# Optimization experiments

Hardware: AMD Instinct MI355X
Metric: run time of the kernel (lower is better)

Reference implementation:

```python
import jax, jax.numpy as jnp
from jax import lax
import numpy as np

D_MODEL = 1024
EXP = 2
D_INNER = EXP * D_MODEL
D_STATE = 16
D_CONV = 4
DT_RANK = 64  # ceil(d_model/16), mamba default
NUM_GROUPS = 4
BSZ, SEQ = 2, 2048
EPS = 1e-5


def setup_inputs() -> dict:
    key = jax.random.key(0)
    ks = jax.random.split(key, 10)
    def n(k, shape, s=0.02):
        return jax.random.normal(k, shape, jnp.float32) * s
    return dict(
        x=jax.random.normal(ks[0], (BSZ, SEQ, D_MODEL), jnp.float32),
        ln1_g=jnp.ones((D_MODEL,), jnp.float32), ln1_b=jnp.zeros((D_MODEL,), jnp.float32),
        ln2_g=jnp.ones((D_MODEL,), jnp.float32), ln2_b=jnp.zeros((D_MODEL,), jnp.float32),
        W1=n(ks[1], (EXP * D_MODEL, D_MODEL)), b1=jnp.zeros((EXP * D_MODEL,), jnp.float32),
        W2=n(ks[2], (D_MODEL, EXP * D_MODEL)), b2=jnp.zeros((D_MODEL,), jnp.float32),
        in_proj_w=n(ks[3], (2 * D_INNER, D_MODEL)),
        conv_w=n(ks[4], (D_INNER, 1, D_CONV), 0.2), conv_b=jnp.zeros((D_INNER,), jnp.float32),
        x_proj_w=n(ks[5], (DT_RANK + 2 * D_STATE, D_INNER)),
        dt_proj_w=n(ks[6], (D_INNER, DT_RANK), 0.1), dt_proj_b=n(ks[7], (D_INNER,), 0.5),
        A_log=jnp.tile(jnp.log(jnp.arange(1, D_STATE + 1, dtype=jnp.float32)), (D_INNER, 1)),
        D_param=jnp.ones((D_INNER,), jnp.float32),
        out_proj_w=n(ks[8], (D_MODEL, D_INNER)),
    )


def _layernorm(x, g, b):
    m = jnp.mean(x, -1, keepdims=True)
    v = jnp.var(x, -1, keepdims=True)
    return (x - m) * lax.rsqrt(v + EPS) * g + b


def _ste_sign(w):
    # sign quantization with straight-through estimator (groupwise split is a no-op for sign)
    return w + lax.stop_gradient(jnp.sign(w) - w)


def _quant_act_groupwise(x, b=8):
    # groups along seq dim (x.shape[1]); gamma is the abs-max over the whole group slab
    Qb = float(2 ** (b - 1))
    B_, L, D = x.shape
    g = x.reshape(B_, NUM_GROUPS, L // NUM_GROUPS, D)
    gamma = jnp.max(jnp.abs(g), axis=(0, 2, 3), keepdims=True)
    q = jnp.clip(g * Qb / (gamma + EPS), -Qb + EPS, Qb - EPS)
    return q.reshape(B_, L, D)


def _mamba(u, in_proj_w, conv_w, conv_b, x_proj_w, dt_proj_w, dt_proj_b, A_log, D_param, out_proj_w):
    B_, L, _ = u.shape
    xz = u @ in_proj_w.T                         # [B, L, 2*d_inner]
    xs, z = jnp.split(xz, 2, axis=-1)
    # depthwise causal conv1d
    xt = jnp.transpose(xs, (0, 2, 1))            # [B, d_inner, L]
    xt = lax.conv_general_dilated(xt, conv_w, (1,), [(D_CONV - 1, 0)],
                                  feature_group_count=D_INNER,
                                  dimension_numbers=('NCH', 'OIH', 'NCH'))
    xt = xt + conv_b[None, :, None]
    xs = jax.nn.silu(jnp.transpose(xt, (0, 2, 1)))  # [B, L, d_inner]
    x_dbl = xs @ x_proj_w.T                      # [B, L, dt_rank + 2*d_state]
    dt, Bm, Cm = jnp.split(x_dbl, [DT_RANK, DT_RANK + D_STATE], axis=-1)
    dt = jax.nn.softplus(dt @ dt_proj_w.T + dt_proj_b)   # [B, L, d_inner]
    A = -jnp.exp(A_log)                          # [d_inner, d_state]

    def step(h, inp):
        dt_s, B_s, C_s, x_s = inp                # [B,di], [B,ds], [B,ds], [B,di]
        dA = jnp.exp(dt_s[..., None] * A)        # [B, di, ds]
        h = h * dA + (dt_s * x_s)[..., None] * B_s[:, None, :]
        y = jnp.einsum('bds,bs->bd', h, C_s)
        return h, y

    tm = lambda a: jnp.transpose(a, (1, 0, 2))   # time-major
    h0 = jnp.zeros((B_, D_INNER, D_STATE), u.dtype)
    _, ys = lax.scan(step, h0, (tm(dt), tm(Bm), tm(Cm), tm(xs)))
    y = jnp.transpose(ys, (1, 0, 2)) + D_param * xs
    y = y * jax.nn.silu(z)
    return y @ out_proj_w.T


def reference(x, ln1_g, ln1_b, ln2_g, ln2_b, W1, b1, W2, b2,
              in_proj_w, conv_w, conv_b, x_proj_w, dt_proj_w, dt_proj_b,
              A_log, D_param, out_proj_w):
    qW1 = _ste_sign(W1)
    qW2 = _ste_sign(W2)
    gated = jnp.clip(_layernorm(x, ln1_g, ln1_b) @ qW1.T + b1, -1.0, 1.0)  # Hardtanh
    x = x + gated @ qW2.T + b2
    qx = _quant_act_groupwise(x)
    out = qx + _mamba(_layernorm(qx, ln2_g, ln2_b), in_proj_w, conv_w, conv_b,
                      x_proj_w, dt_proj_w, dt_proj_b, A_log, D_param, out_proj_w)
    return out
```

## Files before the change

kernel.cpp:

```cpp
#include <hip/hip_runtime.h>
#include <math.h>

#define D_MODEL 1024
#define D_INNER 2048
#define D_STATE 16
#define DT_RANK 64
#define BSZ 2
#define SEQ 2048
#define NTOK (BSZ*SEQ)
#define NCH  (BSZ*D_INNER)
#define NCHUNK 64
#define CLEN 32
#define EPS 1e-5f

typedef __attribute__((ext_vector_type(8))) short short8v;
typedef __attribute__((ext_vector_type(4))) float f32x4;

__device__ __forceinline__ float sgnf(float w) {
    return (w > 0.f) ? 1.f : ((w < 0.f) ? -1.f : 0.f);
}
__device__ __forceinline__ unsigned short f2bf(float f) {
    unsigned int x = __float_as_uint(f);
    x += 0x7fffu + ((x >> 16) & 1u);
    return (unsigned short)(x >> 16);
}
__device__ __forceinline__ float bf2f(unsigned short u) {
    return __uint_as_float(((unsigned int)u) << 16);
}
__device__ __forceinline__ void stage16(const unsigned short* g, unsigned short* l) {
    __builtin_amdgcn_global_load_lds(
        (const __attribute__((address_space(1))) unsigned int*)g,
        (__attribute__((address_space(3))) unsigned int*)l, 16, 0, 0);
}

#define F4_C1   524288
#define F4_C2   1048576
#define F4_C3   2097152
#define F4_C4   2146304
#define F4_C5   2179072
#define F4_C6   2703360
__global__ __launch_bounds__(256) void f2bf_all_kernel(
    const float* __restrict__ W1, const float* __restrict__ W2,
    const float* __restrict__ inpj, const float* __restrict__ xpj,
    const float* __restrict__ dtpj, const float* __restrict__ outpj,
    unsigned short* __restrict__ o_w1, unsigned short* __restrict__ o_w2,
    unsigned short* __restrict__ o_in, unsigned short* __restrict__ o_xp,
    unsigned short* __restrict__ o_dt, unsigned short* __restrict__ o_out,
    unsigned int* __restrict__ gma)
{
    int i = blockIdx.x * 256 + threadIdx.x;
    if (blockIdx.x == 0 && threadIdx.x < 4) gma[threadIdx.x] = 0u;
    if (i >= F4_C6) return;
    const float* src; unsigned short* dst; int off; bool sign = false;
    if (i < F4_C1)      { src = W1;   dst = o_w1;  off = i;          sign = true; }
    else if (i < F4_C2) { src = W2;   dst = o_w2;  off = i - F4_C1;  sign = true; }
    else if (i < F4_C3) { src = inpj; dst = o_in;  off = i - F4_C2; }
    else if (i < F4_C4) { src = xpj;  dst = o_xp;  off = i - F4_C3; }
    else if (i < F4_C5) { src = dtpj; dst = o_dt;  off = i - F4_C4; }
    else                { src = outpj;dst = o_out; off = i - F4_C5; }
    float4 v = reinterpret_cast<const float4*>(src)[off];
    if (sign) { v.x = sgnf(v.x); v.y = sgnf(v.y); v.z = sgnf(v.z); v.w = sgnf(v.w); }
    ushort4 o;
    o.x = f2bf(v.x); o.y = f2bf(v.y); o.z = f2bf(v.z); o.w = f2bf(v.w);
    reinterpret_cast<ushort4*>(dst)[off] = o;
}

__global__ __launch_bounds__(256) void ln_hilo_kernel(const float* __restrict__ x,
                                                      const float* __restrict__ g,
                                                      const float* __restrict__ b,
                                                      unsigned short* __restrict__ hi,
                                                      unsigned short* __restrict__ lo) {
    int row = blockIdx.x, tid = threadIdx.x;
    float4 v = reinterpret_cast<const float4*>(x + (size_t)row * D_MODEL)[tid];
    float s = v.x + v.y + v.z + v.w;
    float q = v.x*v.x + v.y*v.y + v.z*v.z + v.w*v.w;
    #pragma unroll
    for (int off = 32; off > 0; off >>= 1) { s += __shfl_down(s, off); q += __shfl_down(q, off); }
    __shared__ float rs[4], rq[4], smean, srstd;
    if ((tid & 63) == 0) { rs[tid >> 6] = s; rq[tid >> 6] = q; }
    __syncthreads();
    if (tid == 0) {
        float ts = rs[0]+rs[1]+rs[2]+rs[3], tq = rq[0]+rq[1]+rq[2]+rq[3];
        float mean = ts * (1.0f / D_MODEL);
        smean = mean;
        srstd = rsqrtf(tq * (1.0f / D_MODEL) - mean*mean + EPS);
    }
    __syncthreads();
    float mean = smean, rstd = srstd;
    float4 gg = reinterpret_cast<const float4*>(g)[tid];
    float4 bb = reinterpret_cast<const float4*>(b)[tid];
    float o[4];
    o[0] = (v.x-mean)*rstd*gg.x + bb.x; o[1] = (v.y-mean)*rstd*gg.y + bb.y;
    o[2] = (v.z-mean)*rstd*gg.z + bb.z; o[3] = (v.w-mean)*rstd*gg.w + bb.w;
    ushort4 h4, l4;
    h4.x = f2bf(o[0]); l4.x = f2bf(o[0] - bf2f(h4.x));
    h4.y = f2bf(o[1]); l4.y = f2bf(o[1] - bf2f(h4.y));
    h4.z = f2bf(o[2]); l4.z = f2bf(o[2] - bf2f(h4.z));
    h4.w = f2bf(o[3]); l4.w = f2bf(o[3] - bf2f(h4.w));
    reinterpret_cast<ushort4*>(hi + (size_t)row * D_MODEL)[tid] = h4;
    reinterpret_cast<ushort4*>(lo + (size_t)row * D_MODEL)[tid] = l4;
}

template<int EP, bool DUALA, int BN, bool KSPLIT>
__global__ __launch_bounds__(256) void mfma_gemm(
    const unsigned short* __restrict__ A, const unsigned short* __restrict__ A2,
    const unsigned short* __restrict__ B, float* __restrict__ C,
    unsigned short* __restrict__ Cb,
    int M, int N, int K, int sA, int sC,
    const float* __restrict__ bias, const float* __restrict__ addx, int sAdd,
    unsigned int* __restrict__ gma, int ksl)
{
    constexpr int NF = BN / 32;
    __shared__ __align__(16) unsigned short As[128*32];
    __shared__ __align__(16) unsigned short As2[DUALA ? 128*32 : 8];
    __shared__ __align__(16) unsigned short Bs[BN*32];
    __shared__ float redmax[4];
    const int tid = threadIdx.x;
    const int lane = tid & 63;
    const int w = tid >> 6;
    const int wm = w >> 1, wn = w & 1;

    int bx = blockIdx.x, by = blockIdx.y;
    if (!KSPLIT) {
        const int gx = gridDim.x;
        const int nwg = gx * gridDim.y;
        int lin = by * gx + bx;
        int nl = (lin & 7) * (nwg >> 3) + (lin >> 3);
        bx = nl % gx; by = nl / gx;
    }
    const int row0 = by * 128, col0 = bx * BN;
    const int srow = lane >> 2;
    const int scol = (lane & 3) * 8;

    int k_begin = 0, k_end = K;
    if (KSPLIT) {
        int z = blockIdx.z;
        k_begin = z * ksl; k_end = k_begin + ksl;
        C += (size_t)z * M * sC;
    }

    f32x4 acc[4][NF];
    #pragma unroll
    for (int m = 0; m < 4; ++m)
        #pragma unroll
        for (int n = 0; n < NF; ++n)
            acc[m][n] = (f32x4){0.f, 0.f, 0.f, 0.f};

    for (int k0 = k_begin; k0 < k_end; k0 += 32) {
        #pragma unroll
        for (int i = 0; i < 2; ++i) {
            const int rbase = w * 32 + i * 16;
            stage16(A + (size_t)(row0 + rbase + srow) * sA + k0 + scol, &As[rbase * 32]);
            if (DUALA)
                stage16(A2 + (size_t)(row0 + rbase + srow) * sA + k0 + scol, &As2[rbase * 32]);
        }
        #pragma unroll
        for (int i = 0; i < BN/64; ++i) {
            const int rbase = (BN == 128) ? (w * 32 + i * 16) : (w * 16);
            if (col0 + rbase < N)
                stage16(B + (size_t)(col0 + rbase + srow) * K + k0 + scol, &Bs[rbase * 32]);
        }
        __syncthreads();

        short8v af[4], bfr[NF], af2[4];
        const int fr = lane & 15, kg = (lane >> 4) * 8;
        #pragma unroll
        for (int m = 0; m < 4; ++m)
            af[m] = *reinterpret_cast<const short8v*>(&As[(wm*64 + m*16 + fr) * 32 + kg]);
        if (DUALA) {
            #pragma unroll
            for (int m = 0; m < 4; ++m)
                af2[m] = *reinterpret_cast<const short8v*>(&As2[(wm*64 + m*16 + fr) * 32 + kg]);
        }
        #pragma unroll
        for (int n = 0; n < NF; ++n)
            bfr[n] = *reinterpret_cast<const short8v*>(&Bs[(wn*(BN/2) + n*16 + fr) * 32 + kg]);

        #pragma unroll
        for (int m = 0; m < 4; ++m)
            #pragma unroll
            for (int n = 0; n < NF; ++n) {
                acc[m][n] = __builtin_amdgcn_mfma_f32_16x16x32_bf16(af[m], bfr[n], acc[m][n], 0, 0, 0);
                if (DUALA)
                    acc[m][n] = __builtin_amdgcn_mfma_f32_16x16x32_bf16(af2[m], bfr[n], acc[m][n], 0, 0, 0);
            }
        __syncthreads();
    }

    const int fc = lane & 15, r4 = (lane >> 4) * 4;
    float lmax = 0.0f;
    #pragma unroll
    for (int m = 0; m < 4; ++m) {
        const int grb = row0 + wm*64 + m*16 + r4;
        #pragma unroll
        for (int n = 0; n < NF; ++n) {
            const int gc = col0 + wn*(BN/2) + n*16 + fc;
            if (gc >= N) continue;
            #pragma unroll
            for (int j = 0; j < 4; ++j) {
                const int r = grb + j;
                float v = acc[m][n][j];
                if (EP == 0) {
                    C[(size_t)r*sC + gc] = v;
                } else if (EP == 1) {
                    v += bias[gc];
                    v = fminf(1.0f, fmaxf(-1.0f, v));
                    Cb[(size_t)r*sC + gc] = f2bf(v);
                } else if (EP == 3) {
                    float t = v + bias[gc];
                    t = fmaxf(t, 0.0f) + log1pf(__expf(-fabsf(t)));
                    Cb[(size_t)r*sC + gc] = f2bf(t);
                } else if (EP == 4) {
                    C[(size_t)r*sC + gc] = v + addx[(size_t)r*sAdd + gc];
                } else if (EP == 6) {
                    Cb[(size_t)r*sC + gc] = f2bf(v);
                } else {
                    v += bias[gc] + addx[(size_t)r*sAdd + gc];
                    C[(size_t)r*sC + gc] = v;
                    lmax = fmaxf(lmax, fabsf(v));
                }
            }
        }
    }
    if (EP == 7) {
        #pragma unroll
        for (int off = 32; off > 0; off >>= 1) lmax = fmaxf(lmax, __shfl_down(lmax, off));
        if (lane == 0) redmax[w] = lmax;
        __syncthreads();
        if (tid == 0) {
            float t = fmaxf(fmaxf(redmax[0], redmax[1]), fmaxf(redmax[2], redmax[3]));
            int g = (row0 & (SEQ - 1)) >> 9;
            atomicMax(gma + g, __float_as_uint(t));
        }
    }
}

__global__ __launch_bounds__(256) void xproj_combine_kernel(
    const float* __restrict__ part,
    float* __restrict__ xdbl,
    unsigned short* __restrict__ xdt)
{
    int i = blockIdx.x * 256 + threadIdx.x;
    if (i >= NTOK * 24) return;
    const size_t stride = (size_t)NTOK * 96 / 4;
    float4 v0 = reinterpret_cast<const float4*>(part)[i];
    float4 v1 = reinterpret_cast<const float4*>(part)[i + stride];
    float4 v2 = reinterpret_cast<const float4*>(part)[i + 2*stride];
    float4 v3 = reinterpret_cast<const float4*>(part)[i + 3*stride];
    float4 o;
    o.x = (v0.x + v1.x) + (v2.x + v3.x);
    o.y = (v0.y + v1.y) + (v2.y + v3.y);
    o.z = (v0.z + v1.z) + (v2.z + v3.z);
    o.w = (v0.w + v1.w) + (v2.w + v3.w);
    reinterpret_cast<float4*>(xdbl)[i] = o;
    int row = i / 24, c4 = i % 24;
    if (c4 < 16) {
        ushort4 u;
        u.x = f2bf(o.x); u.y = f2bf(o.y); u.z = f2bf(o.z); u.w = f2bf(o.w);
        reinterpret_cast<ushort4*>(xdt + (size_t)row * 64)[c4] = u;
    }
}

__global__ __launch_bounds__(256) void quant_ln_kernel(
    const float* __restrict__ x2, const unsigned int* __restrict__ gamma_bits,
    const float* __restrict__ g, const float* __restrict__ b,
    float* __restrict__ qx, unsigned short* __restrict__ u)
{
    int row = blockIdx.x, tid = threadIdx.x;
    int grp = (row & (SEQ - 1)) >> 9;
    float gamma = __uint_as_float(gamma_bits[grp]);
    float scale = 128.0f / (gamma + EPS);
    const float lo = -128.0f + EPS, hi = 128.0f - EPS;
    float4 v = reinterpret_cast<const float4*>(x2 + (size_t)row * D_MODEL)[tid];
    float4 qv;
    qv.x = fminf(hi, fmaxf(lo, v.x * scale));
    qv.y = fminf(hi, fmaxf(lo, v.y * scale));
    qv.z = fminf(hi, fmaxf(lo, v.z * scale));
    qv.w = fminf(hi, fmaxf(lo, v.w * scale));
    reinterpret_cast<float4*>(qx + (size_t)row * D_MODEL)[tid] = qv;
    float s = qv.x + qv.y + qv.z + qv.w;
    float q = qv.x*qv.x + qv.y*qv.y + qv.z*qv.z + qv.w*qv.w;
    #pragma unroll
    for (int off = 32; off > 0; off >>= 1) { s += __shfl_down(s, off); q += __shfl_down(q, off); }
    __shared__ float rs[4], rq[4], smean, srstd;
    if ((tid & 63) == 0) { rs[tid >> 6] = s; rq[tid >> 6] = q; }
    __syncthreads();
    if (tid == 0) {
        float ts = rs[0]+rs[1]+rs[2]+rs[3], tq = rq[0]+rq[1]+rq[2]+rq[3];
        float mean = ts * (1.0f / D_MODEL);
        smean = mean;
        srstd = rsqrtf(tq * (1.0f / D_MODEL) - mean*mean + EPS);
    }
    __syncthreads();
    float mean = smean, rstd = srstd;
    float4 gg = reinterpret_cast<const float4*>(g)[tid];
    float4 bb = reinterpret_cast<const float4*>(b)[tid];
    ushort4 o;
    o.x = f2bf((qv.x-mean)*rstd*gg.x + bb.x);
    o.y = f2bf((qv.y-mean)*rstd*gg.y + bb.y);
    o.z = f2bf((qv.z-mean)*rstd*gg.z + bb.z);
    o.w = f2bf((qv.w-mean)*rstd*gg.w + bb.w);
    reinterpret_cast<ushort4*>(u + (size_t)row * D_MODEL)[tid] = o;
}

__global__ __launch_bounds__(256) void conv_silu_kernel(const unsigned short* __restrict__ xz,
                                                        const float* __restrict__ conv_w,
                                                        const float* __restrict__ conv_b,
                                                        unsigned short* __restrict__ xcb) {
    int c = blockIdx.x * 256 + threadIdx.x;
    int m = blockIdx.y;
    int b = m >> 11, l = m & (SEQ - 1);
    float4 w4 = reinterpret_cast<const float4*>(conv_w)[c];
    float wv[4] = {w4.x, w4.y, w4.z, w4.w};
    float s = conv_b[c];
    const unsigned short* base = xz + ((size_t)b * SEQ) * 4096 + c;
    #pragma unroll
    for (int k = 0; k < 4; ++k) {
        int ll = l - 3 + k;
        if (ll >= 0) s += bf2f(base[(size_t)ll * 4096]) * wv[k];
    }
    float sig = 1.0f / (1.0f + __expf(-s));
    xcb[(size_t)m * D_INNER + c] = f2bf(s * sig);
}

__device__ __forceinline__ void make_dA(float dA[D_STATE], float dtv,
                                        const float* a, bool pw) {
    if (pw) {
        dA[0] = __expf(dtv * a[0]);
        #pragma unroll
        for (int s = 1; s < D_STATE; ++s) dA[s] = dA[s>>1] * dA[(s-1)>>1];
    } else {
        #pragma unroll
        for (int s = 0; s < D_STATE; ++s) dA[s] = __expf(dtv * a[s]);
    }
}

__global__ __launch_bounds__(256) void scan_partial_kernel(
    const unsigned short* __restrict__ dt, const unsigned short* __restrict__ xcb,
    const float* __restrict__ xdbl, const float* __restrict__ A_log,
    float* __restrict__ Lbuf, float* __restrict__ Sbuf)
{
    int gtid = blockIdx.x * 256 + threadIdx.x;
    int ch = gtid & (NCH - 1);
    int c  = gtid >> 12;
    int b = ch >> 11, d = ch & (D_INNER - 1);
    float a[D_STATE], h[D_STATE];
    bool pw = true;
    #pragma unroll
    for (int s = 0; s < D_STATE; ++s) {
        a[s] = -__expf(A_log[(size_t)d * D_STATE + s]);
        h[s] = 0.0f;
    }
    #pragma unroll
    for (int s = 1; s < D_STATE; ++s)
        pw = pw && (fabsf(a[s] - a[0]*(float)(s+1)) <= 1e-3f * fabsf(a[s]));

    size_t m0 = (size_t)b * SEQ + (size_t)c * CLEN;
    float Ssum = 0.0f;

    float dt_n = bf2f(dt[m0 * D_INNER + d]);
    float x_n  = bf2f(xcb[m0 * D_INNER + d]);
    float4 B_n[4];
    {
        const float* xd = xdbl + m0 * 96;
        #pragma unroll
        for (int i = 0; i < 4; ++i)
            B_n[i] = *reinterpret_cast<const float4*>(xd + DT_RANK + 4*i);
    }

    for (int l = 0; l < CLEN; ++l) {
        float dtv = dt_n, xv = x_n;
        float Bc[D_STATE];
        #pragma unroll
        for (int i = 0; i < 4; ++i) {
            Bc[4*i+0] = B_n[i].x; Bc[4*i+1] = B_n[i].y; Bc[4*i+2] = B_n[i].z; Bc[4*i+3] = B_n[i].w;
        }
        if (l + 1 < CLEN) {
            size_t m1 = m0 + l + 1;
            dt_n = bf2f(dt[m1 * D_INNER + d]);
            x_n  = bf2f(xcb[m1 * D_INNER + d]);
            const float* xd = xdbl + m1 * 96;
            #pragma unroll
            for (int i = 0; i < 4; ++i)
                B_n[i] = *reinterpret_cast<const float4*>(xd + DT_RANK + 4*i);
        }
        Ssum += dtv;
        float dx = dtv * xv;
        float dA[D_STATE];
        make_dA(dA, dtv, a, pw);
        #pragma unroll
        for (int s = 0; s < D_STATE; ++s)
            h[s] = h[s] * dA[s] + dx * Bc[s];
    }
    float4* Lp = reinterpret_cast<float4*>(Lbuf + (size_t)c * (NCH * D_STATE) + (size_t)ch * D_STATE);
    Lp[0] = make_float4(h[0], h[1], h[2], h[3]);
    Lp[1] = make_float4(h[4], h[5], h[6], h[7]);
    Lp[2] = make_float4(h[8], h[9], h[10], h[11]);
    Lp[3] = make_float4(h[12], h[13], h[14], h[15]);
    Sbuf[(size_t)c * NCH + ch] = Ssum;
}

__global__ __launch_bounds__(256) void scan_combine_kernel(
    float* __restrict__ LH, const float* __restrict__ Sbuf,
    const float* __restrict__ A_log)
{
    int gtid = blockIdx.x * 256 + threadIdx.x;
    int s = gtid & (D_STATE - 1);
    int ch = gtid >> 4;
    int d = ch & (D_INNER - 1);
    float a = -__expf(A_log[(size_t)d * D_STATE + s]);
    float h = 0.0f;
    #pragma unroll 4
    for (int c = 0; c < NCHUNK; ++c) {
        size_t idx = (size_t)c * (NCH * D_STATE) + (size_t)ch * D_STATE + s;
        float loc = LH[idx];
        LH[idx] = h;
        float P = __expf(a * Sbuf[(size_t)c * NCH + ch]);
        h = h * P + loc;
    }
}

__global__ __launch_bounds__(256) void scan_final_kernel(
    const unsigned short* __restrict__ dt, const unsigned short* __restrict__ xcb,
    const unsigned short* __restrict__ xzb, const float* __restrict__ xdbl,
    const float* __restrict__ A_log, const float* __restrict__ D_param,
    const float* __restrict__ Hin, unsigned short* __restrict__ yb)
{
    int gtid = blockIdx.x * 256 + threadIdx.x;
    int ch = gtid & (NCH - 1);
    int c  = gtid >> 12;
    int b = ch >> 11, d = ch & (D_INNER - 1);
    float a[D_STATE], h[D_STATE];
    {
        const float4* Hp = reinterpret_cast<const float4*>(
            Hin + (size_t)c * (NCH * D_STATE) + (size_t)ch * D_STATE);
        float4 h0 = Hp[0], h1 = Hp[1], h2 = Hp[2], h3 = Hp[3];
        h[0]=h0.x; h[1]=h0.y; h[2]=h0.z; h[3]=h0.w;
        h[4]=h1.x; h[5]=h1.y; h[6]=h1.z; h[7]=h1.w;
        h[8]=h2.x; h[9]=h2.y; h[10]=h2.z; h[11]=h2.w;
        h[12]=h3.x; h[13]=h3.y; h[14]=h3.z; h[15]=h3.w;
    }
    bool pw = true;
    #pragma unroll
    for (int s = 0; s < D_STATE; ++s)
        a[s] = -__expf(A_log[(size_t)d * D_STATE + s]);
    #pragma unroll
    for (int s = 1; s < D_STATE; ++s)
        pw = pw && (fabsf(a[s] - a[0]*(float)(s+1)) <= 1e-3f * fabsf(a[s]));
    float Dp = D_param[d];

    size_t m0 = (size_t)b * SEQ + (size_t)c * CLEN;
    float dt_n = bf2f(dt[m0 * D_INNER + d]);
    float x_n  = bf2f(xcb[m0 * D_INNER + d]);
    float z_n  = bf2f(xzb[m0 * 4096 + D_INNER + d]);
    float4 B_n[4], C_n[4];
    {
        const float* xd = xdbl + m0 * 96;
        #pragma unroll
        for (int i = 0; i < 4; ++i) {
            B_n[i] = *reinterpret_cast<const float4*>(xd + DT_RANK + 4*i);
            C_n[i] = *reinterpret_cast<const float4*>(xd + DT_RANK + D_STATE + 4*i);
        }
    }

    for (int l = 0; l < CLEN; ++l) {
        float dtv = dt_n, xv = x_n, zv = z_n;
        float Bc[D_STATE], Cc[D_STATE];
        #pragma unroll
        for (int i = 0; i < 4; ++i) {
            Bc[4*i+0] = B_n[i].x; Bc[4*i+1] = B_n[i].y; Bc[4*i+2] = B_n[i].z; Bc[4*i+3] = B_n[i].w;
            Cc[4*i+0] = C_n[i].x; Cc[4*i+1] = C_n[i].y; Cc[4*i+2] = C_n[i].z; Cc[4*i+3] = C_n[i].w;
        }
        if (l + 1 < CLEN) {
            size_t m1 = m0 + l + 1;
            dt_n = bf2f(dt[m1 * D_INNER + d]);
            x_n  = bf2f(xcb[m1 * D_INNER + d]);
            z_n  = bf2f(xzb[m1 * 4096 + D_INNER + d]);
            const float* xd = xdbl + m1 * 96;
            #pragma unroll
            for (int i = 0; i < 4; ++i) {
                B_n[i] = *reinterpret_cast<const float4*>(xd + DT_RANK + 4*i);
                C_n[i] = *reinterpret_cast<const float4*>(xd + DT_RANK + D_STATE + 4*i);
            }
        }
        float dx = dtv * xv;
        float yv = 0.0f;
        float dA[D_STATE];
        make_dA(dA, dtv, a, pw);
        #pragma unroll
        for (int s = 0; s < D_STATE; ++s) {
            h[s] = h[s] * dA[s] + dx * Bc[s];
            yv += h[s] * Cc[s];
        }
        yv += Dp * xv;
        float sig = 1.0f / (1.0f + __expf(-zv));
        yb[(m0 + l) * D_INNER + d] = f2bf(yv * (zv * sig));
    }
}

extern "C" void kernel_launch(void* const* d_in, const int* in_sizes, int n_in,
                              void* d_out, int out_size, void* d_ws, size_t ws_size,
                              hipStream_t stream) {
    const float* x         = (const float*)d_in[0];
    const float* ln1_g     = (const float*)d_in[1];
    const float* ln1_b     = (const float*)d_in[2];
    const float* ln2_g     = (const float*)d_in[3];
    const float* ln2_b     = (const float*)d_in[4];
    const float* W1        = (const float*)d_in[5];
    const float* b1        = (const float*)d_in[6];
    const float* W2        = (const float*)d_in[7];
    const float* b2        = (const float*)d_in[8];
    const float* in_proj   = (const float*)d_in[9];
    const float* conv_w    = (const float*)d_in[10];
    const float* conv_b    = (const float*)d_in[11];
    const float* x_proj    = (const float*)d_in[12];
    const float* dt_proj   = (const float*)d_in[13];
    const float* dt_proj_b = (const float*)d_in[14];
    const float* A_log     = (const float*)d_in[15];
    const float* D_param   = (const float*)d_in[16];
    const float* out_proj  = (const float*)d_in[17];
    float* out = (float*)d_out;

    char* ws = (char*)d_ws;
    float*          f_x2   = (float*)         (ws + 0);
    unsigned short* b_xz   = (unsigned short*)(ws + 16777216);
    unsigned short* b_dt   = (unsigned short*)(ws + 50331648);
    float*          f_xdbl = (float*)         (ws + 83886080);
    float*          f_L    = (float*)         (ws + 85458944);
    float*          f_xp   = f_L;
    float*          f_S    = (float*)         (ws + 102236160);
    unsigned int*   f_gamma= (unsigned int*)  (ws + 103284736);
    unsigned short* b_a1hi = (unsigned short*)(ws + 103284800);
    unsigned short* b_a1lo = b_a1hi + 4194304;
    unsigned short* b_y    = b_a1hi;
    unsigned short* b_gated= (unsigned short*)(ws + 120062016);
    unsigned short* b_xc   = b_gated;
    unsigned short* b_u    = (unsigned short*)(ws + 136839232);
    unsigned short* b_xdt  = b_u;
    unsigned short* b_w1s  = (unsigned short*)(ws + 145227840);
    unsigned short* b_w2s  = (unsigned short*)(ws + 149422144);
    unsigned short* b_inpj = (unsigned short*)(ws + 153616448);
    unsigned short* b_xpj  = (unsigned short*)(ws + 162005056);
    unsigned short* b_dtpj = (unsigned short*)(ws + 162398272);
    unsigned short* b_outpj= (unsigned short*)(ws + 162660416);

    dim3 b256(256);

    f2bf_all_kernel<<<dim3((F4_C6 + 255)/256), b256, 0, stream>>>(
        W1, W2, in_proj, x_proj, dt_proj, out_proj,
        b_w1s, b_w2s, b_inpj, b_xpj, b_dtpj, b_outpj, f_gamma);

    ln_hilo_kernel<<<dim3(NTOK), b256, 0, stream>>>(x, ln1_g, ln1_b, b_a1hi, b_a1lo);
    mfma_gemm<1, true, 128, false><<<dim3(16, 32), b256, 0, stream>>>(
        b_a1hi, b_a1lo, b_w1s, nullptr, b_gated, NTOK, D_INNER, D_MODEL, D_MODEL, D_INNER,
        b1, nullptr, 0, nullptr, 0);
    mfma_gemm<7, false, 128, false><<<dim3(8, 32), b256, 0, stream>>>(
        b_gated, nullptr, b_w2s, f_x2, nullptr, NTOK, D_MODEL, D_INNER, D_INNER, D_MODEL,
        b2, x, D_MODEL, f_gamma, 0);
    quant_ln_kernel<<<dim3(NTOK), b256, 0, stream>>>(f_x2, f_gamma, ln2_g, ln2_b, f_x2, b_u);
    mfma_gemm<6, false, 128, false><<<dim3(32, 32), b256, 0, stream>>>(
        b_u, nullptr, b_inpj, nullptr, b_xz, NTOK, 2*D_INNER, D_MODEL, D_MODEL, 2*D_INNER,
        nullptr, nullptr, 0, nullptr, 0);
    conv_silu_kernel<<<dim3(D_INNER/256, NTOK), b256, 0, stream>>>(b_xz, conv_w, conv_b, b_xc);
    mfma_gemm<0, false, 128, true><<<dim3(1, 32, 4), b256, 0, stream>>>(
        b_xc, nullptr, b_xpj, f_xp, nullptr, NTOK, DT_RANK + 2*D_STATE, D_INNER, D_INNER,
        DT_RANK + 2*D_STATE, nullptr, nullptr, 0, nullptr, 512);
    xproj_combine_kernel<<<dim3((NTOK*24 + 255)/256), b256, 0, stream>>>(f_xp, f_xdbl, b_xdt);
    mfma_gemm<3, false, 64, false><<<dim3(32, 32), b256, 0, stream>>>(
        b_xdt, nullptr, b_dtpj, nullptr, b_dt, NTOK, D_INNER, DT_RANK, DT_RANK, D_INNER,
        dt_proj_b, nullptr, 0, nullptr, 0);
    scan_partial_kernel<<<dim3(NCH*NCHUNK/256), b256, 0, stream>>>(
        b_dt, b_xc, f_xdbl, A_log, f_L, f_S);
    scan_combine_kernel<<<dim3(NCH*D_STATE/256), b256, 0, stream>>>(f_L, f_S, A_log);
    scan_final_kernel<<<dim3(NCH*NCHUNK/256), b256, 0, stream>>>(
        b_dt, b_xc, b_xz, f_xdbl, A_log, D_param, f_L, b_y);
    mfma_gemm<4, false, 128, false><<<dim3(8, 32), b256, 0, stream>>>(
        b_y, nullptr, b_outpj, out, nullptr, NTOK, D_MODEL, D_INNER, D_INNER, D_MODEL,
        nullptr, f_x2, D_MODEL, nullptr, 0);
}
```

Measured before the change: 473.1 us.

## Use 256x256 double-buffered MFMA GEMM for in_proj

Adds a dedicated 512-thread GEMM kernel with 256x256 output tiles, 64-wide K steps, double-buffered direct-to-LDS staging, XCD-aware block remapping, and interleaved LDS reads with MFMA phases using setprio and barriers. It replaces the generic 128-tile GEMM for the in_proj projection. The goal is more data reuse per tile and better overlap of loads with compute. In exchange it uses 128 KB of LDS and many accumulator registers, and launches only 256 blocks.

```diff
diff --git a/kernel.cpp b/kernel.cpp
--- a/kernel.cpp
+++ b/kernel.cpp
@@ -32,6 +32,7 @@
         (const __attribute__((address_space(1))) unsigned int*)g,
         (__attribute__((address_space(3))) unsigned int*)l, 16, 0, 0);
 }
+#define LDv(p) (*reinterpret_cast<const short8v*>(p))
 
 #define F4_C1   524288
 #define F4_C2   1048576
@@ -101,6 +102,143 @@
     reinterpret_cast<ushort4*>(lo + (size_t)row * D_MODEL)[tid] = l4;
 }
 
+__global__ __launch_bounds__(512) void mfma_gemm256_bf16out(
+    const unsigned short* __restrict__ A, const unsigned short* __restrict__ B,
+    unsigned short* __restrict__ Cb, int M, int N, int K, int sA, int sC)
+{
+    __shared__ __align__(16) unsigned short As[2][256*64];
+    __shared__ __align__(16) unsigned short Bs[2][256*64];
+    const int tid = threadIdx.x, lane = tid & 63, w = tid >> 6;
+    const int wm = w >> 2, wn = w & 3;
+    int bx = blockIdx.x, by = blockIdx.y;
+    {
+        const int gx = gridDim.x, nwg = gx * gridDim.y;
+        int lin = by * gx + bx;
+        int nl = (lin & 7) * (nwg >> 3) + (lin >> 3);
+        bx = nl % gx; by = nl / gx;
+    }
+    const int row0 = by * 256, col0 = bx * 256;
+    const int lr = lane >> 3, lc = lane & 7;
+    const int ga = wn;
+    const int h2 = wn >> 1, g2 = wm * 2 + (wn & 1);
+    const int T = K >> 6;
+
+    f32x4 acc[8][4];
+    #pragma unroll
+    for (int m = 0; m < 8; ++m)
+        #pragma unroll
+        for (int n = 0; n < 4; ++n) acc[m][n] = (f32x4){0.f,0.f,0.f,0.f};
+
+    auto STAGE = [&](int t) {
+        const int kk = t << 6, p = t & 1;
+        #pragma unroll
+        for (int i = 0; i < 4; ++i) {
+            const int rl = wm*128 + ga*32 + i*8;
+            stage16(A + (size_t)(row0 + rl + lr) * sA + kk + lc*8, &As[p][rl*64]);
+        }
+        #pragma unroll
+        for (int i = 0; i < 4; ++i) {
+            const int rl = h2*128 + g2*32 + i*8;
+            stage16(B + (size_t)(col0 + rl + lr) * K + kk + lc*8, &Bs[p][rl*64]);
+        }
+    };
+
+    STAGE(0); STAGE(1);
+
+    const int fr = lane & 15, kg = (lane >> 4) * 8;
+
+    for (int t = 0; t < T; ++t) {
+        const int p = t & 1;
+        if (t + 1 < T) asm volatile("s_waitcnt vmcnt(8)" ::: "memory");
+        else           asm volatile("s_waitcnt vmcnt(0)" ::: "memory");
+        __builtin_amdgcn_sched_barrier(0);
+        __builtin_amdgcn_s_barrier();
+
+        const unsigned short* Ab = &As[p][(wm*128 + fr) * 64 + kg];
+        const unsigned short* Bb = &Bs[p][(wn*64  + fr) * 64 + kg];
+        short8v aX[4][2], bX[2][2], bY[2][2];
+
+        #pragma unroll
+        for (int m = 0; m < 4; ++m) {
+            aX[m][0] = LDv(Ab + m*16*64);
+            aX[m][1] = LDv(Ab + m*16*64 + 32);
+        }
+        #pragma unroll
+        for (int n = 0; n < 2; ++n) {
+            bX[n][0] = LDv(Bb + n*16*64);
+            bX[n][1] = LDv(Bb + n*16*64 + 32);
+        }
+        __builtin_amdgcn_s_barrier();
+        __builtin_amdgcn_s_setprio(1);
+        #pragma unroll
+        for (int m = 0; m < 4; ++m)
+            #pragma unroll
+            for (int n = 0; n < 2; ++n) {
+                acc[m][n] = __builtin_amdgcn_mfma_f32_16x16x32_bf16(aX[m][0], bX[n][0], acc[m][n],0,0,0);
+                acc[m][n] = __builtin_amdgcn_mfma_f32_16x16x32_bf16(aX[m][1], bX[n][1], acc[m][n],0,0,0);
+            }
+        __builtin_amdgcn_s_setprio(0);
+        __builtin_amdgcn_s_barrier();
+        #pragma unroll
+        for (int n = 0; n < 2; ++n) {
+            bY[n][0] = LDv(Bb + (n+2)*16*64);
+            bY[n][1] = LDv(Bb + (n+2)*16*64 + 32);
+        }
+        __builtin_amdgcn_s_barrier();
+        __builtin_amdgcn_s_setprio(1);
+        #pragma unroll
+        for (int m = 0; m < 4; ++m)
+            #pragma unroll
+            for (int n = 0; n < 2; ++n) {
+                acc[m][n+2] = __builtin_amdgcn_mfma_f32_16x16x32_bf16(aX[m][0], bY[n][0], acc[m][n+2],0,0,0);
+                acc[m][n+2] = __builtin_amdgcn_mfma_f32_16x16x32_bf16(aX[m][1], bY[n][1], acc[m][n+2],0,0,0);
+            }
+        __builtin_amdgcn_s_setprio(0);
+        __builtin_amdgcn_s_barrier();
+        #pragma unroll
+        for (int m = 0; m < 4; ++m) {
+            aX[m][0] = LDv(Ab + (m+4)*16*64);
+            aX[m][1] = LDv(Ab + (m+4)*16*64 + 32);
+        }
+        __builtin_amdgcn_s_barrier();
+        __builtin_amdgcn_s_setprio(1);
+        #pragma unroll
+        for (int m = 0; m < 4; ++m)
+            #pragma unroll
+            for (int n = 0; n < 2; ++n) {
+                acc[m+4][n] = __builtin_amdgcn_mfma_f32_16x16x32_bf16(aX[m][0], bX[n][0], acc[m+4][n],0,0,0);
+                acc[m+4][n] = __builtin_amdgcn_mfma_f32_16x16x32_bf16(aX[m][1], bX[n][1], acc[m+4][n],0,0,0);
+            }
+        __builtin_amdgcn_s_setprio(0);
+        __builtin_amdgcn_s_barrier();
+        if (t + 2 < T) STAGE(t + 2);
+        __builtin_amdgcn_s_barrier();
+        __builtin_amdgcn_s_setprio(1);
+        #pragma unroll
+        for (int m = 0; m < 4; ++m)
+            #pragma unroll
+            for (int n = 0; n < 2; ++n) {
+                acc[m+4][n+2] = __builtin_amdgcn_mfma_f32_16x16x32_bf16(aX[m][0], bY[n][0], acc[m+4][n+2],0,0,0);
+                acc[m+4][n+2] = __builtin_amdgcn_mfma_f32_16x16x32_bf16(aX[m][1], bY[n][1], acc[m+4][n+2],0,0,0);
+            }
+        __builtin_amdgcn_s_setprio(0);
+        __builtin_amdgcn_s_barrier();
+    }
+
+    const int fc = lane & 15, r4 = (lane >> 4) * 4;
+    #pragma unroll
+    for (int m = 0; m < 8; ++m) {
+        const int r = row0 + wm*128 + m*16 + r4;
+        #pragma unroll
+        for (int n = 0; n < 4; ++n) {
+            const int gc = col0 + wn*64 + n*16 + fc;
+            #pragma unroll
+            for (int j = 0; j < 4; ++j)
+                Cb[(size_t)(r + j)*sC + gc] = f2bf(acc[m][n][j]);
+        }
+    }
+}
+
 template<int EP, bool DUALA, int BN, bool KSPLIT>
 __global__ __launch_bounds__(256) void mfma_gemm(
     const unsigned short* __restrict__ A, const unsigned short* __restrict__ A2,
@@ -558,9 +696,8 @@
         b_gated, nullptr, b_w2s, f_x2, nullptr, NTOK, D_MODEL, D_INNER, D_INNER, D_MODEL,
         b2, x, D_MODEL, f_gamma, 0);
     quant_ln_kernel<<<dim3(NTOK), b256, 0, stream>>>(f_x2, f_gamma, ln2_g, ln2_b, f_x2, b_u);
-    mfma_gemm<6, false, 128, false><<<dim3(32, 32), b256, 0, stream>>>(
-        b_u, nullptr, b_inpj, nullptr, b_xz, NTOK, 2*D_INNER, D_MODEL, D_MODEL, 2*D_INNER,
-        nullptr, nullptr, 0, nullptr, 0);
+    mfma_gemm256_bf16out<<<dim3(16, 16), dim3(512), 0, stream>>>(
+        b_u, b_inpj, b_xz, NTOK, 2*D_INNER, D_MODEL, D_MODEL, 2*D_INNER);
     conv_silu_kernel<<<dim3(D_INNER/256, NTOK), b256, 0, stream>>>(b_xz, conv_w, conv_b, b_xc);
     mfma_gemm<0, false, 128, true><<<dim3(1, 32, 4), b256, 0, stream>>>(
         b_xc, nullptr, b_xpj, f_xp, nullptr, NTOK, DT_RANK + 2*D_STATE, D_INNER, D_INNER,
```

Measured after the change: 476.7 us. About the same (+0.8%).
